# Optimization experiments

Measured on AMD Instinct MI355X. Metric: run time of the kernel, lower is better.

The kernel has to match this reference:

```python
import jax, jax.numpy as jnp
import numpy as np
from jax.ops import segment_sum, segment_max

N, E, P = 3072, 147456, 100000
IN_CH, HID, HEADS, LAYERS = 128, 256, 4, 2
WL, RWSE_DIM = 16, 16
DH = HID // HEADS


def setup_inputs() -> dict:
    key = jax.random.key(0)
    ks = jax.random.split(key, 16)
    s = 0.05
    return {
        "x": jax.random.normal(ks[0], (N, IN_CH), jnp.float32),
        "edge_index": jax.random.randint(ks[1], (2, E), 0, N, jnp.int32),
        "src": jax.random.randint(ks[2], (P,), 0, N, jnp.int32),
        "dst": jax.random.randint(ks[3], (P,), 0, N, jnp.int32),
        "rwse_w": jax.random.normal(ks[4], (WL, RWSE_DIM), jnp.float32) * s,
        "rwse_b": jnp.zeros((RWSE_DIM,), jnp.float32),
        "proj_w": jax.random.normal(ks[5], (IN_CH + RWSE_DIM, HID), jnp.float32) * s,
        "proj_b": jnp.zeros((HID,), jnp.float32),
        "Wq": jax.random.normal(ks[6], (LAYERS, HID, HID), jnp.float32) * s,
        "bq": jnp.zeros((LAYERS, HID), jnp.float32),
        "Wk": jax.random.normal(ks[7], (LAYERS, HID, HID), jnp.float32) * s,
        "bk": jnp.zeros((LAYERS, HID), jnp.float32),
        "Wv": jax.random.normal(ks[8], (LAYERS, HID, HID), jnp.float32) * s,
        "bv": jnp.zeros((LAYERS, HID), jnp.float32),
        "Ws": jax.random.normal(ks[9], (LAYERS, HID, HID), jnp.float32) * s,
        "bs": jnp.zeros((LAYERS, HID), jnp.float32),
        "ln_g": jnp.ones((LAYERS, HID), jnp.float32),
        "ln_b": jnp.zeros((LAYERS, HID), jnp.float32),
    }


def _layernorm(h, g, b):
    mu = h.mean(-1, keepdims=True)
    var = ((h - mu) ** 2).mean(-1, keepdims=True)
    return (h - mu) * jax.lax.rsqrt(var + 1e-5) * g + b


def reference(x, edge_index, src, dst, rwse_w, rwse_b, proj_w, proj_b,
              Wq, bq, Wk, bk, Wv, bv, Ws, bs, ln_g, ln_b):
    n = x.shape[0]
    # --- RWSE positional encoding (dense random-walk diagonals) ---
    adj = jnp.zeros((n, n), x.dtype).at[edge_index[0], edge_index[1]].add(1.0)
    deg = jnp.clip(adj.sum(axis=1, keepdims=True), 1.0, None)
    rw = adj / deg  # row-normalized transition matrix

    def step(power, _):
        power = power @ rw
        return power, jnp.diagonal(power)

    _, diags = jax.lax.scan(step, jnp.eye(n, dtype=x.dtype), None, length=WL)
    pe = diags.T @ rwse_w + rwse_b  # [n, RWSE_DIM]

    # --- input projection ---
    h = jnp.concatenate([x, pe], axis=-1) @ proj_w + proj_b  # [n, HID]

    sidx, tidx = edge_index[0], edge_index[1]  # message j -> i (source, target)
    scale = 1.0 / np.sqrt(DH)
    for l in range(LAYERS):
        q = (h @ Wq[l] + bq[l]).reshape(n, HEADS, DH)
        k = (h @ Wk[l] + bk[l]).reshape(n, HEADS, DH)
        v = (h @ Wv[l] + bv[l]).reshape(n, HEADS, DH)
        # per-edge attention logits [E, HEADS]
        score = (q[tidx] * k[sidx]).sum(-1) * scale
        # segment softmax over incoming edges of each target node
        m = segment_max(score, tidx, num_segments=n)
        m = jnp.where(jnp.isfinite(m), m, 0.0)
        e = jnp.exp(score - m[tidx])
        denom = segment_sum(e, tidx, num_segments=n)
        alpha = e / jnp.maximum(denom[tidx], 1e-16)
        agg = segment_sum(alpha[:, :, None] * v[sidx], tidx, num_segments=n)
        out = agg.reshape(n, HID) + h @ Ws[l] + bs[l]  # attn + root skip (lin_skip)
        h = jax.nn.relu(_layernorm(h + out, ln_g[l], ln_b[l]))

    # --- dot-product link decode ---
    return jax.nn.sigmoid((h[src] * h[dst]).sum(-1))
```

## Files before the change

### kernel.cpp

```cpp
#include <hip/hip_runtime.h>
#include <hip/hip_bf16.h>
#include <hip/hip_fp8.h>

#define NN   3072
#define NE   147456
#define NP   100000
#define HID  256
#define INCH 128
#define CATK 144
#define KPAD 160
#define FP8_S    1024.0f
#define FP8_IS   (1.0f / 1024.0f)
#define FP8_IS2  (1.0f / (1024.0f * 1024.0f))
#define MAXE 128

typedef __attribute__((ext_vector_type(4))) float    f32x4;
typedef __attribute__((ext_vector_type(8))) _Float16 f16x8;
typedef __attribute__((ext_vector_type(4))) _Float16 f16x4;
typedef __attribute__((ext_vector_type(8))) unsigned char u8x8;
typedef __attribute__((ext_vector_type(4))) int i32x4;
typedef __attribute__((ext_vector_type(8))) int i32x8;

__device__ __forceinline__ float fp8f(unsigned char b) {
  __hip_fp8_e4m3 t; t.__x = b; return (float)t;
}
__device__ __forceinline__ unsigned char f2fp8(float v) {
  __hip_fp8_e4m3 t(v); return t.__x;
}

__device__ __forceinline__ void gload16(const void* g, void* l) {
  __builtin_amdgcn_global_load_lds((const __attribute__((address_space(1))) void*)g,
                                   (__attribute__((address_space(3))) void*)l, 16, 0, 0);
}

__global__ void prep_kernel(const int* __restrict__ ei, float* __restrict__ adj,
                            int* __restrict__ cnt,
                            const float* __restrict__ proj_w, _Float16* __restrict__ wt_proj,
                            const float* __restrict__ Wq, const float* __restrict__ Wk,
                            const float* __restrict__ Wv, const float* __restrict__ Wsk,
                            const float* __restrict__ bq, const float* __restrict__ bk,
                            const float* __restrict__ bv, const float* __restrict__ bsk,
                            _Float16* __restrict__ wt_cat0, _Float16* __restrict__ wt_cat1,
                            float* __restrict__ bcat0, float* __restrict__ bcat1) {
  int bid = blockIdx.x, tid = threadIdx.x;
  if (bid < 576) {
    int e = bid * 256 + tid;
    if (e < NE) {
      int s = ei[e], t = ei[NE + e];
      atomicAdd(&adj[(size_t)s * NN + t], 1.0f);
      atomicAdd(&cnt[t], 1);
    }
    return;
  }
  if (bid < 736) {
    int idx = (bid - 576) * 256 + tid;
    if (idx < HID * KPAD) {
      int n = idx / KPAD, k = idx - n * KPAD;
      wt_proj[idx] = (k < CATK) ? (_Float16)proj_w[(size_t)k * HID + n] : (_Float16)0.f;
    }
    return;
  }
  int l = (bid < 1760) ? 0 : 1;
  int idx = (bid - (l ? 1760 : 736)) * 256 + tid;
  const float* Wq_ = Wq + (size_t)l * HID * HID;
  const float* Wk_ = Wk + (size_t)l * HID * HID;
  const float* Wv_ = Wv + (size_t)l * HID * HID;
  const float* Ws_ = Wsk + (size_t)l * HID * HID;
  _Float16* wt = l ? wt_cat1 : wt_cat0;
  float* bcat = l ? bcat1 : bcat0;
  if (idx < 1024) {
    int s = idx >> 8, j = idx & 255;
    bcat[idx] = (s == 0) ? bq[l * HID + j] : (s == 1) ? bk[l * HID + j]
              : (s == 2) ? bv[l * HID + j] : bsk[l * HID + j];
  }
  if (idx < 4 * HID * HID) {
    int nrow = idx >> 8, k = idx & 255;
    int s = nrow >> 8, nc = nrow & 255;
    const float* W = (s == 0) ? Wq_ : (s == 1) ? Wk_ : (s == 2) ? Wv_ : Ws_;
    wt[idx] = (_Float16)W[(size_t)k * HID + nc];
  }
}

__global__ void rownorm_scan_kernel(const float* __restrict__ adj, unsigned char* __restrict__ rw,
                                    float* __restrict__ diag1,
                                    const int* __restrict__ cnt, int* __restrict__ off) {
  int bid = blockIdx.x, tid = threadIdx.x;
  if (bid < NN) {
    const float* ap = adj + (size_t)bid * NN;
    float s = 0.f;
    for (int j = tid; j < NN; j += 256) s += ap[j];
    for (int d = 32; d; d >>= 1) s += __shfl_xor(s, d);
    __shared__ float w4[4];
    if ((tid & 63) == 0) w4[tid >> 6] = s;
    __syncthreads();
    float inv = 1.f / fmaxf(w4[0] + w4[1] + w4[2] + w4[3], 1.f);
    unsigned char* rp = rw + (size_t)bid * NN;
    for (int j = tid; j < NN; j += 256) {
      float v = ap[j] * inv;
      rp[j] = f2fp8(v * FP8_S);
      if (j == bid) diag1[bid] = v;
    }
    return;
  }
  if (tid >= 64) return;
  int lane = tid;
  const int per = NN / 64;
  int s = 0;
  for (int i = 0; i < per; i++) s += cnt[lane * per + i];
  int run = s;
  for (int d = 1; d < 64; d <<= 1) {
    int t = __shfl_up(run, d);
    if (lane >= d) run += t;
  }
  int acc = run - s;
  for (int i = 0; i < per; i++) {
    off[lane * per + i] = acc;
    acc += cnt[lane * per + i];
  }
  if (lane == 63) off[NN] = acc;
}

__device__ __forceinline__ void transpose_body(const unsigned char* __restrict__ in,
                                               unsigned char* __restrict__ out,
                                               int bx, int by, int tid) {
  __shared__ unsigned char t[64][68];
#pragma unroll
  for (int ii = 0; ii < 4; ii++) {
    int lin = ii * 256 + tid;
    int r = lin >> 4, c4 = (lin & 15) * 4;
    unsigned int v = *(const unsigned int*)(in + (size_t)(by * 64 + r) * NN + bx * 64 + c4);
    t[r][c4] = v & 255; t[r][c4 + 1] = (v >> 8) & 255;
    t[r][c4 + 2] = (v >> 16) & 255; t[r][c4 + 3] = v >> 24;
  }
  __syncthreads();
#pragma unroll
  for (int ii = 0; ii < 4; ii++) {
    int lin = ii * 256 + tid;
    int r = lin >> 4, c4 = (lin & 15) * 4;
    unsigned int v = (unsigned int)t[c4][r] | ((unsigned int)t[c4 + 1][r] << 8) |
                     ((unsigned int)t[c4 + 2][r] << 16) | ((unsigned int)t[c4 + 3][r] << 24);
    *(unsigned int*)(out + (size_t)(bx * 64 + r) * NN + by * 64 + c4) = v;
  }
}

__global__ void fill_transpose_kernel(const int* __restrict__ sidx, const int* __restrict__ tidx,
                                      const int* __restrict__ off, int* __restrict__ cur,
                                      int* __restrict__ csrc,
                                      const unsigned char* __restrict__ rw,
                                      unsigned char* __restrict__ rwT) {
  int bid = blockIdx.x, tid = threadIdx.x;
  if (bid < 576) {
    int e = bid * 256 + tid;
    if (e < NE) {
      int t = tidx[e];
      int pos = atomicAdd(&cur[t], 1);
      csrc[off[t] + pos] = sidx[e];
    }
    return;
  }
  int t = bid - 576;
  transpose_body(rw, rwT, t % 48, t / 48, tid);
}

__global__ void transpose3_kernel(const unsigned char* __restrict__ rw4, unsigned char* __restrict__ rw4T,
                                  const unsigned char* __restrict__ rw2, unsigned char* __restrict__ rw2T,
                                  const unsigned char* __restrict__ rw3, unsigned char* __restrict__ rw3T) {
  const unsigned char* in  = (blockIdx.z == 0) ? rw4  : (blockIdx.z == 1) ? rw2  : rw3;
  unsigned char* out       = (blockIdx.z == 0) ? rw4T : (blockIdx.z == 1) ? rw2T : rw3T;
  transpose_body(in, out, blockIdx.x, blockIdx.y, threadIdx.x);
}

__global__ __launch_bounds__(256) void gemm_fp8_nt(const unsigned char* __restrict__ A,
                                                   const unsigned char* __restrict__ Bt,
                                                   unsigned char* __restrict__ C, int n) {
  __shared__ __align__(16) unsigned char As[128 * 128];
  __shared__ __align__(16) unsigned char Bs[128 * 128];
  const int nbx = n >> 7;
  const int nb = nbx * nbx;
  const int bid = blockIdx.x;
  const int cpx = nb >> 3;
  const int wg = (bid & 7) * cpx + (bid >> 3);
  const int by = wg / nbx, bx = wg % nbx;
  const int tid = threadIdx.x;
  const int lane = tid & 63, wave = tid >> 6;
  const int wr = wave >> 1, wc = wave & 1;
  const int rowA0 = by * 128, rowB0 = bx * 128;
  const int fr = lane & 15;
  const int kg = lane >> 4;
  const int sr = tid >> 3;
  const int scd = tid & 7;
  f32x4 acc[4][4] = {};
  const int nkt = n >> 7;
  for (int kt = 0; kt < nkt; ++kt) {
    const int k0 = kt << 7;
#pragma unroll
    for (int s = 0; s < 4; s++) {
      const int row = sr + s * 32;
      const int cg = (scd ^ (row & 7)) << 4;
      gload16(A + (size_t)(rowA0 + row) * n + k0 + cg, As + row * 128 + scd * 16);
      gload16(Bt + (size_t)(rowB0 + row) * n + k0 + cg, Bs + row * 128 + scd * 16);
    }
    __syncthreads();
    i32x8 af[4], bf[4];
#pragma unroll
    for (int i = 0; i < 4; i++) {
      const int Ra = wr * 64 + i * 16 + fr;
      const int Rb = wc * 64 + i * 16 + fr;
      const int c0a = ((2 * kg) ^ (Ra & 7)) << 4, c1a = ((2 * kg + 1) ^ (Ra & 7)) << 4;
      const int c0b = ((2 * kg) ^ (Rb & 7)) << 4, c1b = ((2 * kg + 1) ^ (Rb & 7)) << 4;
      i32x4 alo = *(const i32x4*)(As + Ra * 128 + c0a);
      i32x4 ahi = *(const i32x4*)(As + Ra * 128 + c1a);
      i32x4 blo = *(const i32x4*)(Bs + Rb * 128 + c0b);
      i32x4 bhi = *(const i32x4*)(Bs + Rb * 128 + c1b);
      af[i] = (i32x8){alo[0], alo[1], alo[2], alo[3], ahi[0], ahi[1], ahi[2], ahi[3]};
      bf[i] = (i32x8){blo[0], blo[1], blo[2], blo[3], bhi[0], bhi[1], bhi[2], bhi[3]};
    }
#pragma unroll
    for (int i = 0; i < 4; i++)
#pragma unroll
      for (int j = 0; j < 4; j++)
        acc[i][j] = __builtin_amdgcn_mfma_scale_f32_16x16x128_f8f6f4(
            af[i], bf[j], acc[i][j], 0, 0, 0, 127, 0, 127);
    __syncthreads();
  }
  const int crow0 = rowA0 + wr * 64, ccol0 = rowB0 + wc * 64;
#pragma unroll
  for (int i = 0; i < 4; i++)
#pragma unroll
    for (int j = 0; j < 4; j++)
#pragma unroll
      for (int r = 0; r < 4; r++) {
        int row = crow0 + i * 16 + (lane >> 4) * 4 + r;
        int col = ccol0 + j * 16 + (lane & 15);
        C[(size_t)row * n + col] = f2fp8(acc[i][j][r] * FP8_IS);
      }
}

__global__ __launch_bounds__(256) void diag_all_kernel(
    const unsigned char* __restrict__ rw, const unsigned char* __restrict__ rw2,
    const unsigned char* __restrict__ rw4, const unsigned char* __restrict__ rw8,
    const unsigned char* __restrict__ rw12, const unsigned char* __restrict__ rwT,
    const unsigned char* __restrict__ rw2T, const unsigned char* __restrict__ rw3T,
    const unsigned char* __restrict__ rw4T, float* __restrict__ diags) {
  int row = blockIdx.x, tid = threadIdx.x;
  size_t base = (size_t)row * NN;
  const u8x8* pl1  = (const u8x8*)(rw + base);
  const u8x8* pl2  = (const u8x8*)(rw2 + base);
  const u8x8* pl4  = (const u8x8*)(rw4 + base);
  const u8x8* pl8  = (const u8x8*)(rw8 + base);
  const u8x8* pl12 = (const u8x8*)(rw12 + base);
  const u8x8* pr1  = (const u8x8*)(rwT + base);
  const u8x8* pr2  = (const u8x8*)(rw2T + base);
  const u8x8* pr3  = (const u8x8*)(rw3T + base);
  const u8x8* pr4  = (const u8x8*)(rw4T + base);
  float s[15];
#pragma unroll
  for (int k = 0; k < 15; k++) s[k] = 0.f;
  for (int j = tid; j < NN / 8; j += 256) {
    u8x8 L1 = pl1[j], L2 = pl2[j], L4 = pl4[j], L8 = pl8[j], L12 = pl12[j];
    u8x8 R1 = pr1[j], R2 = pr2[j], R3 = pr3[j], R4 = pr4[j];
#pragma unroll
    for (int r = 0; r < 8; r++) {
      float a1 = fp8f(L1[r]), a2 = fp8f(L2[r]), a4 = fp8f(L4[r]),
            a8 = fp8f(L8[r]), a12 = fp8f(L12[r]);
      float b1 = fp8f(R1[r]), b2 = fp8f(R2[r]), b3 = fp8f(R3[r]), b4 = fp8f(R4[r]);
      s[0]  += a1 * b1;  s[1]  += a2 * b1;  s[2]  += a2 * b2;
      s[3]  += a4 * b1;  s[4]  += a4 * b2;  s[5]  += a4 * b3;  s[6]  += a4 * b4;
      s[7]  += a8 * b1;  s[8]  += a8 * b2;  s[9]  += a8 * b3;  s[10] += a8 * b4;
      s[11] += a12 * b1; s[12] += a12 * b2; s[13] += a12 * b3; s[14] += a12 * b4;
    }
  }
  __shared__ float red[15][4];
  int wave = tid >> 6, lane = tid & 63;
#pragma unroll
  for (int k = 0; k < 15; k++) {
    float v = s[k];
    for (int d = 32; d; d >>= 1) v += __shfl_xor(v, d);
    if (lane == 0) red[k][wave] = v;
  }
  __syncthreads();
  if (tid < 15)
    diags[(size_t)(tid + 1) * NN + row] =
        (red[tid][0] + red[tid][1] + red[tid][2] + red[tid][3]) * FP8_IS2;
}

__global__ __launch_bounds__(256) void gemm_f16_node(const _Float16* __restrict__ A,
                                                     const _Float16* __restrict__ Bt,
                                                     const float* __restrict__ bias,
                                                     const _Float16* __restrict__ addhi,
                                                     _Float16* __restrict__ C16,
                                                     int M, int Nn, int K) {
  __shared__ _Float16 As[64 * 32];
  __shared__ _Float16 Bs[64 * 32];
  const int tid = threadIdx.x;
  const int lane = tid & 63, wave = tid >> 6;
  const int wr = wave >> 1, wc = wave & 1;
  const int m0 = blockIdx.y * 64, n0 = blockIdx.x * 64;
  const int fr = lane & 15, fk = (lane >> 4) * 8;
  const int gr = tid >> 2, gc = (tid & 3) * 8;
  f32x4 acc[2][2] = {};
  for (int k0 = 0; k0 < K; k0 += 32) {
    gload16(A + (size_t)(m0 + gr) * K + k0 + gc, As + tid * 8);
    gload16(Bt + (size_t)(n0 + gr) * K + k0 + gc, Bs + tid * 8);
    __syncthreads();
    f16x8 af[2], bf[2];
#pragma unroll
    for (int i = 0; i < 2; i++) {
      af[i] = *(const f16x8*)(As + (wr * 32 + i * 16 + fr) * 32 + fk);
      bf[i] = *(const f16x8*)(Bs + (wc * 32 + i * 16 + fr) * 32 + fk);
    }
#pragma unroll
    for (int i = 0; i < 2; i++)
#pragma unroll
      for (int j = 0; j < 2; j++)
        acc[i][j] = __builtin_amdgcn_mfma_f32_16x16x32_f16(af[i], bf[j], acc[i][j], 0, 0, 0);
    __syncthreads();
  }
  const int crow0 = m0 + wr * 32, ccol0 = n0 + wc * 32;
#pragma unroll
  for (int i = 0; i < 2; i++)
#pragma unroll
    for (int j = 0; j < 2; j++)
#pragma unroll
      for (int r = 0; r < 4; r++) {
        int row = crow0 + i * 16 + (lane >> 4) * 4 + r;
        int col = ccol0 + j * 16 + (lane & 15);
        float val = acc[i][j][r];
        if (bias) val += bias[col];
        if (addhi && col >= Nn - 256) val += (float)addhi[(size_t)row * 256 + col - (Nn - 256)];
        C16[(size_t)row * Nn + col] = (_Float16)val;
      }
}

__global__ void concat16_kernel(const float* __restrict__ x, const float* __restrict__ diags,
                                const float* __restrict__ w, const float* __restrict__ bb,
                                _Float16* __restrict__ xc) {
  int idx = blockIdx.x * 256 + threadIdx.x;
  if (idx >= NN * KPAD) return;
  int i = idx / KPAD, c = idx - i * KPAD;
  float v;
  if (c < INCH) v = x[(size_t)i * INCH + c];
  else if (c < CATK) {
    int d = c - INCH;
    v = bb[d];
#pragma unroll
    for (int t = 0; t < 16; t++) v += diags[t * NN + i] * w[t * 16 + d];
  } else v = 0.f;
  xc[idx] = (_Float16)v;
}

__global__ __launch_bounds__(256) void attn_ln_kernel(const int* __restrict__ off,
                                                      const int* __restrict__ csrc,
                                                      const _Float16* __restrict__ qkvz,
                                                      const float* __restrict__ g,
                                                      const float* __restrict__ b,
                                                      _Float16* __restrict__ h16) {
  int node = blockIdx.x, tid = threadIdx.x;
  int h = tid >> 6, lane = tid & 63;
  int beg = off[node], end = off[node + 1];
  __shared__ _Float16 qs[256];
  __shared__ int srcs[MAXE];
  __shared__ float ps[4][MAXE];
  qs[tid] = qkvz[(size_t)node * 1024 + tid];
  float m_run = -INFINITY, d_run = 0.f, acc = 0.f;
  for (int chunk = beg; chunk < end; chunk += MAXE) {
    int ne = min(end - chunk, MAXE);
    if (tid < ne) srcs[tid] = csrc[chunk + tid];
    __syncthreads();
    for (int p = tid; p < ne * 4; p += 256) {
      int e = p >> 2, h2 = p & 3;
      const f16x8* krow = (const f16x8*)(qkvz + (size_t)srcs[e] * 1024 + 256 + h2 * 64);
      const f16x8* qrow = (const f16x8*)(qs + h2 * 64);
      float sc = 0.f;
#pragma unroll
      for (int d8 = 0; d8 < 8; d8++) {
        f16x8 kv = krow[d8], qv = qrow[d8];
#pragma unroll
        for (int r = 0; r < 8; r++) sc += (float)qv[r] * (float)kv[r];
      }
      ps[h2][e] = sc * 0.125f;
    }
    __syncthreads();
    float mloc = -INFINITY;
    for (int e = lane; e < ne; e += 64) mloc = fmaxf(mloc, ps[h][e]);
    for (int d = 32; d; d >>= 1) mloc = fmaxf(mloc, __shfl_xor(mloc, d));
    float mnew = fmaxf(m_run, mloc);
    float dloc = 0.f;
    for (int e = lane; e < ne; e += 64) {
      float p = __expf(ps[h][e] - mnew);
      ps[h][e] = p;
      dloc += p;
    }
    for (int d = 32; d; d >>= 1) dloc += __shfl_xor(dloc, d);
    float scale = __expf(m_run - mnew);
    d_run = d_run * scale + dloc;
    acc *= scale;
    const size_t vb = 512 + (size_t)h * 64 + lane;
    int e = 0;
    for (; e + 4 <= ne; e += 4) {
      float v0 = (float)qkvz[(size_t)srcs[e]     * 1024 + vb];
      float v1 = (float)qkvz[(size_t)srcs[e + 1] * 1024 + vb];
      float v2 = (float)qkvz[(size_t)srcs[e + 2] * 1024 + vb];
      float v3 = (float)qkvz[(size_t)srcs[e + 3] * 1024 + vb];
      acc += ps[h][e] * v0 + ps[h][e + 1] * v1 + ps[h][e + 2] * v2 + ps[h][e + 3] * v3;
    }
    for (; e < ne; ++e)
      acc += ps[h][e] * (float)qkvz[(size_t)srcs[e] * 1024 + vb];
    m_run = mnew;
    __syncthreads();
  }
  float agg = acc / fmaxf(d_run, 1e-16f);
  float z = (float)qkvz[(size_t)node * 1024 + 768 + tid] + agg;
  float s = z;
  for (int d = 32; d; d >>= 1) s += __shfl_xor(s, d);
  __shared__ float w4[4], w4b[4];
  if (lane == 0) w4[h] = s;
  __syncthreads();
  float mu = (w4[0] + w4[1] + w4[2] + w4[3]) * (1.f / HID);
  float dv = z - mu;
  float qv = dv * dv;
  for (int d = 32; d; d >>= 1) qv += __shfl_xor(qv, d);
  if (lane == 0) w4b[h] = qv;
  __syncthreads();
  float var = (w4b[0] + w4b[1] + w4b[2] + w4b[3]) * (1.f / HID);
  float y = dv * (1.f / sqrtf(var + 1e-5f)) * g[tid] + b[tid];
  y = fmaxf(y, 0.f);
  h16[(size_t)node * HID + tid] = (_Float16)y;
}

__global__ void decode_kernel(const _Float16* __restrict__ h, const int* __restrict__ src,
                              const int* __restrict__ dst, float* __restrict__ out) {
  int wv = threadIdx.x >> 6, lane = threadIdx.x & 63;
  int p = blockIdx.x * 4 + wv;
  if (p >= NP) return;
  const f16x4* a = (const f16x4*)(h + (size_t)src[p] * HID);
  const f16x4* b = (const f16x4*)(h + (size_t)dst[p] * HID);
  f16x4 x = a[lane], y = b[lane];
  float s = (float)x[0] * (float)y[0] + (float)x[1] * (float)y[1] +
            (float)x[2] * (float)y[2] + (float)x[3] * (float)y[3];
  for (int d = 32; d; d >>= 1) s += __shfl_xor(s, d);
  if (lane == 0) out[p] = 1.f / (1.f + expf(-s));
}

extern "C" void kernel_launch(void* const* d_in, const int* in_sizes, int n_in,
                              void* d_out, int out_size, void* d_ws, size_t ws_size,
                              hipStream_t stream) {
  const float* x      = (const float*)d_in[0];
  const int*   ei     = (const int*)d_in[1];
  const int*   src    = (const int*)d_in[2];
  const int*   dst    = (const int*)d_in[3];
  const float* rwse_w = (const float*)d_in[4];
  const float* rwse_b = (const float*)d_in[5];
  const float* proj_w = (const float*)d_in[6];
  const float* proj_b = (const float*)d_in[7];
  const float* Wq     = (const float*)d_in[8];
  const float* bq     = (const float*)d_in[9];
  const float* Wk     = (const float*)d_in[10];
  const float* bk     = (const float*)d_in[11];
  const float* Wv     = (const float*)d_in[12];
  const float* bv     = (const float*)d_in[13];
  const float* Wsk    = (const float*)d_in[14];
  const float* bs     = (const float*)d_in[15];
  const float* ln_g   = (const float*)d_in[16];
  const float* ln_b   = (const float*)d_in[17];
  float* out = (float*)d_out;

  const size_t M8 = (size_t)NN * NN;
  char* base = (char*)d_ws;
  unsigned char* rw   = (unsigned char*)(base + 0 * M8);
  unsigned char* rwT  = (unsigned char*)(base + 1 * M8);
  unsigned char* rw2  = (unsigned char*)(base + 2 * M8);
  unsigned char* rw3  = (unsigned char*)(base + 3 * M8);
  unsigned char* rw4  = (unsigned char*)(base + 4 * M8);
  unsigned char* rw4T = (unsigned char*)(base + 5 * M8);
  unsigned char* rw8  = (unsigned char*)(base + 6 * M8);
  unsigned char* rw12 = (unsigned char*)(base + 7 * M8);
  unsigned char* rw2T = (unsigned char*)(base + 8 * M8);
  unsigned char* rw3T = (unsigned char*)(base + 9 * M8);
  float* adj = (float*)(base + 6 * M8);
  char* sm = base + 10 * M8;
  float* diags = (float*)sm; sm += (size_t)16 * NN * 4;
  int* cnt = (int*)sm; sm += 12288;
  int* cur = (int*)sm; sm += 12288;
  int* off = (int*)sm; sm += 16384;
  int* csrc = (int*)sm; sm += (size_t)NE * 4;
  _Float16* qkvz16 = (_Float16*)sm; sm += (size_t)NN * 1024 * 2;
  _Float16* h16  = (_Float16*)sm; sm += (size_t)NN * HID * 2;
  _Float16* xc16 = (_Float16*)sm; sm += (size_t)NN * KPAD * 2;
  _Float16* wt_proj = (_Float16*)sm; sm += (size_t)HID * KPAD * 2;
  _Float16* wt_cat[2]; float* bcat[2];
  for (int l = 0; l < 2; ++l) {
    wt_cat[l] = (_Float16*)sm; sm += (size_t)4 * HID * HID * 2;
    bcat[l]   = (float*)sm;    sm += 1024 * 4;
  }
  (void)in_sizes; (void)n_in; (void)out_size; (void)ws_size;

  const dim3 B256(256);
  const dim3 gT3(NN / 64, NN / 64, 3);
  const int  gG = (NN / 128) * (NN / 128);
  const dim3 gW(1024 / 64, NN / 64);
  const dim3 gS(HID / 64, NN / 64);

  hipMemsetAsync(adj, 0, (size_t)NN * NN * 4, stream);
  hipMemsetAsync(cnt, 0, 24576, stream);

  prep_kernel<<<2784, B256, 0, stream>>>(ei, adj, cnt, proj_w, wt_proj,
                                         Wq, Wk, Wv, Wsk, bq, bk, bv, bs,
                                         wt_cat[0], wt_cat[1], bcat[0], bcat[1]);
  rownorm_scan_kernel<<<NN + 1, B256, 0, stream>>>(adj, rw, diags, cnt, off);
  fill_transpose_kernel<<<576 + 2304, B256, 0, stream>>>(ei, ei + NE, off, cur, csrc, rw, rwT);

  gemm_fp8_nt<<<gG, B256, 0, stream>>>(rw, rwT, rw2, NN);
  gemm_fp8_nt<<<gG, B256, 0, stream>>>(rw2, rwT, rw3, NN);
  gemm_fp8_nt<<<gG, B256, 0, stream>>>(rw3, rwT, rw4, NN);
  transpose3_kernel<<<gT3, B256, 0, stream>>>(rw4, rw4T, rw2, rw2T, rw3, rw3T);
  gemm_fp8_nt<<<gG, B256, 0, stream>>>(rw4, rw4T, rw8, NN);
  gemm_fp8_nt<<<gG, B256, 0, stream>>>(rw8, rw4T, rw12, NN);
  diag_all_kernel<<<NN, B256, 0, stream>>>(rw, rw2, rw4, rw8, rw12,
                                           rwT, rw2T, rw3T, rw4T, diags);

  concat16_kernel<<<(NN * KPAD + 255) / 256, B256, 0, stream>>>(x, diags, rwse_w, rwse_b, xc16);
  gemm_f16_node<<<gS, B256, 0, stream>>>(xc16, wt_proj, proj_b, nullptr, h16, NN, HID, KPAD);

  for (int l = 0; l < 2; ++l) {
    gemm_f16_node<<<gW, B256, 0, stream>>>(h16, wt_cat[l], bcat[l], h16, qkvz16,
                                           NN, 1024, HID);
    attn_ln_kernel<<<NN, B256, 0, stream>>>(off, csrc, qkvz16, ln_g + l * HID, ln_b + l * HID,
                                            h16);
  }

  decode_kernel<<<NP / 4, B256, 0, stream>>>(h16, src, dst, out);
}
```

Measured before the change: 500.8 us.

## Double FP8 GEMM K-tile to 256, fuse diag with concat, merge memsets

The FP8 power-matrix GEMM now stages a 256-wide K slice per iteration (32KB LDS per operand) with a 16-way XOR swizzle. This halves the barrier and loop count, and each sync is followed by two MFMA sub-steps. The diagonal reduction kernel now also computes the RWSE projection and writes the concatenated fp16 input row, which removes a separate concat kernel and the diag round trip through global memory. The two memsets are merged into one, which relies on cnt sitting contiguously after the adj region. The cost is more LDS per block, 64KB, which may lower occupancy.

```diff
diff --git a/kernel.cpp b/kernel.cpp
--- a/kernel.cpp
+++ b/kernel.cpp
@@ -173,8 +173,8 @@
 __global__ __launch_bounds__(256) void gemm_fp8_nt(const unsigned char* __restrict__ A,
                                                    const unsigned char* __restrict__ Bt,
                                                    unsigned char* __restrict__ C, int n) {
-  __shared__ __align__(16) unsigned char As[128 * 128];
-  __shared__ __align__(16) unsigned char Bs[128 * 128];
+  __shared__ __align__(16) unsigned char As[128 * 256];
+  __shared__ __align__(16) unsigned char Bs[128 * 256];
   const int nbx = n >> 7;
   const int nb = nbx * nbx;
   const int bid = blockIdx.x;
@@ -187,40 +187,44 @@
   const int rowA0 = by * 128, rowB0 = bx * 128;
   const int fr = lane & 15;
   const int kg = lane >> 4;
-  const int sr = tid >> 3;
-  const int scd = tid & 7;
+  const int sr = tid >> 4;
+  const int scd = tid & 15;
   f32x4 acc[4][4] = {};
-  const int nkt = n >> 7;
+  const int nkt = n >> 8;
   for (int kt = 0; kt < nkt; ++kt) {
-    const int k0 = kt << 7;
-#pragma unroll
-    for (int s = 0; s < 4; s++) {
-      const int row = sr + s * 32;
-      const int cg = (scd ^ (row & 7)) << 4;
-      gload16(A + (size_t)(rowA0 + row) * n + k0 + cg, As + row * 128 + scd * 16);
-      gload16(Bt + (size_t)(rowB0 + row) * n + k0 + cg, Bs + row * 128 + scd * 16);
-    }
-    __syncthreads();
-    i32x8 af[4], bf[4];
-#pragma unroll
-    for (int i = 0; i < 4; i++) {
-      const int Ra = wr * 64 + i * 16 + fr;
-      const int Rb = wc * 64 + i * 16 + fr;
-      const int c0a = ((2 * kg) ^ (Ra & 7)) << 4, c1a = ((2 * kg + 1) ^ (Ra & 7)) << 4;
-      const int c0b = ((2 * kg) ^ (Rb & 7)) << 4, c1b = ((2 * kg + 1) ^ (Rb & 7)) << 4;
-      i32x4 alo = *(const i32x4*)(As + Ra * 128 + c0a);
-      i32x4 ahi = *(const i32x4*)(As + Ra * 128 + c1a);
-      i32x4 blo = *(const i32x4*)(Bs + Rb * 128 + c0b);
-      i32x4 bhi = *(const i32x4*)(Bs + Rb * 128 + c1b);
-      af[i] = (i32x8){alo[0], alo[1], alo[2], alo[3], ahi[0], ahi[1], ahi[2], ahi[3]};
-      bf[i] = (i32x8){blo[0], blo[1], blo[2], blo[3], bhi[0], bhi[1], bhi[2], bhi[3]};
-    }
-#pragma unroll
-    for (int i = 0; i < 4; i++)
-#pragma unroll
-      for (int j = 0; j < 4; j++)
-        acc[i][j] = __builtin_amdgcn_mfma_scale_f32_16x16x128_f8f6f4(
-            af[i], bf[j], acc[i][j], 0, 0, 0, 127, 0, 127);
+    const int k0 = kt << 8;
+#pragma unroll
+    for (int s = 0; s < 8; s++) {
+      const int row = sr + s * 16;
+      const int cg = (scd ^ (row & 15)) << 4;
+      gload16(A + (size_t)(rowA0 + row) * n + k0 + cg, As + row * 256 + scd * 16);
+      gload16(Bt + (size_t)(rowB0 + row) * n + k0 + cg, Bs + row * 256 + scd * 16);
+    }
+    __syncthreads();
+#pragma unroll
+    for (int sub = 0; sub < 2; sub++) {
+      const int cbase = sub * 8 + 2 * kg;
+      i32x8 af[4], bf[4];
+#pragma unroll
+      for (int i = 0; i < 4; i++) {
+        const int Ra = wr * 64 + i * 16 + fr;
+        const int Rb = wc * 64 + i * 16 + fr;
+        const int c0a = (cbase ^ (Ra & 15)) << 4, c1a = ((cbase + 1) ^ (Ra & 15)) << 4;
+        const int c0b = (cbase ^ (Rb & 15)) << 4, c1b = ((cbase + 1) ^ (Rb & 15)) << 4;
+        i32x4 alo = *(const i32x4*)(As + Ra * 256 + c0a);
+        i32x4 ahi = *(const i32x4*)(As + Ra * 256 + c1a);
+        i32x4 blo = *(const i32x4*)(Bs + Rb * 256 + c0b);
+        i32x4 bhi = *(const i32x4*)(Bs + Rb * 256 + c1b);
+        af[i] = (i32x8){alo[0], alo[1], alo[2], alo[3], ahi[0], ahi[1], ahi[2], ahi[3]};
+        bf[i] = (i32x8){blo[0], blo[1], blo[2], blo[3], bhi[0], bhi[1], bhi[2], bhi[3]};
+      }
+#pragma unroll
+      for (int i = 0; i < 4; i++)
+#pragma unroll
+        for (int j = 0; j < 4; j++)
+          acc[i][j] = __builtin_amdgcn_mfma_scale_f32_16x16x128_f8f6f4(
+              af[i], bf[j], acc[i][j], 0, 0, 0, 127, 0, 127);
+    }
     __syncthreads();
   }
   const int crow0 = rowA0 + wr * 64, ccol0 = rowB0 + wc * 64;
@@ -236,12 +240,14 @@
       }
 }
 
-__global__ __launch_bounds__(256) void diag_all_kernel(
+__global__ __launch_bounds__(256) void diag_concat_kernel(
     const unsigned char* __restrict__ rw, const unsigned char* __restrict__ rw2,
     const unsigned char* __restrict__ rw4, const unsigned char* __restrict__ rw8,
     const unsigned char* __restrict__ rw12, const unsigned char* __restrict__ rwT,
     const unsigned char* __restrict__ rw2T, const unsigned char* __restrict__ rw3T,
-    const unsigned char* __restrict__ rw4T, float* __restrict__ diags) {
+    const unsigned char* __restrict__ rw4T, const float* __restrict__ diag1,
+    const float* __restrict__ x, const float* __restrict__ rwse_w,
+    const float* __restrict__ rwse_b, _Float16* __restrict__ xc) {
   int row = blockIdx.x, tid = threadIdx.x;
   size_t base = (size_t)row * NN;
   const u8x8* pl1  = (const u8x8*)(rw + base);
@@ -271,6 +277,7 @@
     }
   }
   __shared__ float red[15][4];
+  __shared__ float sdiag[16], spe[16];
   int wave = tid >> 6, lane = tid & 63;
 #pragma unroll
   for (int k = 0; k < 15; k++) {
@@ -280,8 +287,21 @@
   }
   __syncthreads();
   if (tid < 15)
-    diags[(size_t)(tid + 1) * NN + row] =
-        (red[tid][0] + red[tid][1] + red[tid][2] + red[tid][3]) * FP8_IS2;
+    sdiag[tid + 1] = (red[tid][0] + red[tid][1] + red[tid][2] + red[tid][3]) * FP8_IS2;
+  if (tid == 15) sdiag[0] = diag1[row];
+  __syncthreads();
+  if (tid < 16) {
+    float v = rwse_b[tid];
+#pragma unroll
+    for (int t = 0; t < 16; t++) v += sdiag[t] * rwse_w[t * 16 + tid];
+    spe[tid] = v;
+  }
+  __syncthreads();
+  if (tid < KPAD) {
+    float v = (tid < INCH) ? x[(size_t)row * INCH + tid]
+            : (tid < CATK ? spe[tid - INCH] : 0.f);
+    xc[(size_t)row * KPAD + tid] = (_Float16)v;
+  }
 }
 
 __global__ __launch_bounds__(256) void gemm_f16_node(const _Float16* __restrict__ A,
@@ -330,23 +350,6 @@
         if (addhi && col >= Nn - 256) val += (float)addhi[(size_t)row * 256 + col - (Nn - 256)];
         C16[(size_t)row * Nn + col] = (_Float16)val;
       }
-}
-
-__global__ void concat16_kernel(const float* __restrict__ x, const float* __restrict__ diags,
-                                const float* __restrict__ w, const float* __restrict__ bb,
-                                _Float16* __restrict__ xc) {
-  int idx = blockIdx.x * 256 + threadIdx.x;
-  if (idx >= NN * KPAD) return;
-  int i = idx / KPAD, c = idx - i * KPAD;
-  float v;
-  if (c < INCH) v = x[(size_t)i * INCH + c];
-  else if (c < CATK) {
-    int d = c - INCH;
-    v = bb[d];
-#pragma unroll
-    for (int t = 0; t < 16; t++) v += diags[t * NN + i] * w[t * 16 + d];
-  } else v = 0.f;
-  xc[idx] = (_Float16)v;
 }
 
 __global__ __launch_bounds__(256) void attn_ln_kernel(const int* __restrict__ off,
@@ -479,11 +482,11 @@
   unsigned char* rw3T = (unsigned char*)(base + 9 * M8);
   float* adj = (float*)(base + 6 * M8);
   char* sm = base + 10 * M8;
-  float* diags = (float*)sm; sm += (size_t)16 * NN * 4;
   int* cnt = (int*)sm; sm += 12288;
   int* cur = (int*)sm; sm += 12288;
   int* off = (int*)sm; sm += 16384;
   int* csrc = (int*)sm; sm += (size_t)NE * 4;
+  float* diag1 = (float*)sm; sm += (size_t)NN * 4;
   _Float16* qkvz16 = (_Float16*)sm; sm += (size_t)NN * 1024 * 2;
   _Float16* h16  = (_Float16*)sm; sm += (size_t)NN * HID * 2;
   _Float16* xc16 = (_Float16*)sm; sm += (size_t)NN * KPAD * 2;
@@ -501,13 +504,12 @@
   const dim3 gW(1024 / 64, NN / 64);
   const dim3 gS(HID / 64, NN / 64);
 
-  hipMemsetAsync(adj, 0, (size_t)NN * NN * 4, stream);
-  hipMemsetAsync(cnt, 0, 24576, stream);
+  hipMemsetAsync(adj, 0, 4 * M8 + 24576, stream);
 
   prep_kernel<<<2784, B256, 0, stream>>>(ei, adj, cnt, proj_w, wt_proj,
                                          Wq, Wk, Wv, Wsk, bq, bk, bv, bs,
                                          wt_cat[0], wt_cat[1], bcat[0], bcat[1]);
-  rownorm_scan_kernel<<<NN + 1, B256, 0, stream>>>(adj, rw, diags, cnt, off);
+  rownorm_scan_kernel<<<NN + 1, B256, 0, stream>>>(adj, rw, diag1, cnt, off);
   fill_transpose_kernel<<<576 + 2304, B256, 0, stream>>>(ei, ei + NE, off, cur, csrc, rw, rwT);
 
   gemm_fp8_nt<<<gG, B256, 0, stream>>>(rw, rwT, rw2, NN);
@@ -516,10 +518,11 @@
   transpose3_kernel<<<gT3, B256, 0, stream>>>(rw4, rw4T, rw2, rw2T, rw3, rw3T);
   gemm_fp8_nt<<<gG, B256, 0, stream>>>(rw4, rw4T, rw8, NN);
   gemm_fp8_nt<<<gG, B256, 0, stream>>>(rw8, rw4T, rw12, NN);
-  diag_all_kernel<<<NN, B256, 0, stream>>>(rw, rw2, rw4, rw8, rw12,
-                                           rwT, rw2T, rw3T, rw4T, diags);
-
-  concat16_kernel<<<(NN * KPAD + 255) / 256, B256, 0, stream>>>(x, diags, rwse_w, rwse_b, xc16);
+
+  diag_concat_kernel<<<NN, B256, 0, stream>>>(rw, rw2, rw4, rw8, rw12,
+                                              rwT, rw2T, rw3T, rw4T, diag1,
+                                              x, rwse_w, rwse_b, xc16);
+
   gemm_f16_node<<<gS, B256, 0, stream>>>(xc16, wt_proj, proj_b, nullptr, h16, NN, HID, KPAD);
 
   for (int l = 0; l < 2; ++l) {
```

New measurement: 543.8 us. +8.6%, slower.
